# Optimization experiments

Measured on AMD Instinct MI355X. Metric: run time of the kernel, lower is better.

The kernel has to match this reference:

```python
import jax, jax.numpy as jnp
import numpy as np

FEATURE_DIM = 256
TEMP = 0.1
BASE_TEMP = 0.07
MAX_SAMPLES = 1024
SIM_THR = 0.7


def setup_inputs() -> dict:
    key = jax.random.key(0)
    ks = jax.random.split(key, 8)
    B, C, H, W = 4, FEATURE_DIM, 160, 160
    s = 1.0 / np.sqrt(C)
    return {
        'feats': jax.random.normal(ks[0], (B, C, H, W), jnp.float32),
        'labels': jax.random.randint(ks[1], (B, H, W), 0, 2).astype(jnp.int64),
        'superpixel_indice': jax.random.randint(ks[2], (B, H, W), 0, 200).astype(jnp.int64),
        'w1': jax.random.normal(ks[3], (C, C), jnp.float32) * s,
        'b1': jnp.zeros((C,), jnp.float32),
        'w2': jax.random.normal(ks[4], (C, C), jnp.float32) * s,
        'b2': jnp.zeros((C,), jnp.float32),
        'wa1': jax.random.normal(ks[5], (64, C), jnp.float32) * s,
        'ba1': jnp.zeros((64,), jnp.float32),
        'wa2': jax.random.normal(ks[6], (1, 64), jnp.float32) * (1.0 / 8.0),
        'ba2': jnp.zeros((1,), jnp.float32),
    }


def _per_sample(f, w, lab, sp):
    # f: (N, C) normalized proj feats, w: (N,) pixel weights, lab/sp: (N,) int
    valid = lab == 1
    # deterministic sample: stable-sort valid pixels to the front, take MAX_SAMPLES
    order = jnp.argsort(jnp.where(valid, 0, 1).astype(jnp.int32))
    idx = order[:MAX_SAMPLES]
    sel = valid[idx]                       # (S,) real-sample mask (pads if <S valid)
    tf = f[idx]                            # (S, C)
    tw = w[idx]                            # (S,)
    ts = sp[idx]                           # (S,)
    sim = tf @ tf.T                        # (S, S)
    S = MAX_SAMPLES
    eye = jnp.eye(S, dtype=bool)
    pos = (ts[:, None] == ts[None, :]) & (sim > SIM_THR)
    pos = pos & sel[:, None] & sel[None, :] & ~eye
    exp_sim = jnp.exp(sim / TEMP) * sel[None, :].astype(sim.dtype)
    denom = exp_sim.sum(axis=1)            # (S,)
    log_prob = sim / TEMP - jnp.log(jnp.where(denom > 0, denom, 1.0))[:, None]
    pw = tw[:, None] * tw[None, :]
    pwm = jnp.where(pos, pw, 0.0)
    psum = pwm.sum()
    loss = -(TEMP / BASE_TEMP) * (pwm * jnp.where(pos, log_prob, 0.0)).sum() / jnp.where(psum > 0, psum, 1.0)
    has = psum > 0
    return jnp.where(has, loss, 0.0), has


def reference(feats, labels, superpixel_indice, w1, b1, w2, b2, wa1, ba1, wa2, ba2):
    B, C, H, W = feats.shape
    x = jnp.transpose(feats, (0, 2, 3, 1)).reshape(B, H * W, C)  # (B, N, C)
    proj = jax.nn.relu(x @ w1.T + b1) @ w2.T + b2                # 1x1 convs == per-pixel matmul
    attn = jax.nn.sigmoid(jax.nn.relu(x @ wa1.T + ba1) @ wa2.T + ba2)[..., 0]  # (B, N)
    nrm = jnp.linalg.norm(proj, axis=-1, keepdims=True)
    fn = proj / jnp.maximum(nrm, 1e-12)
    lab = labels.reshape(B, -1)
    sp = superpixel_indice.reshape(B, -1)
    losses, flags = jax.vmap(_per_sample)(fn, attn, lab, sp)
    n = flags.sum().astype(jnp.float32)
    return jnp.where(n > 0, losses.sum() / jnp.maximum(n, 1.0), 0.0)
```

## Files before the change

### kernel.cpp

```cpp
#include <hip/hip_runtime.h>
#include <hip/hip_bf16.h>
#include <math.h>

#define NPIX   25600
#define CDIM   256
#define SSEL   1024
#define BATCH  4
#define NCHUNK 25
#define INV_T  10.0f
#define RATIO  1.4285714285714286f
#define THR    0.7f

typedef __attribute__((ext_vector_type(8))) short bf16x8;
typedef __attribute__((ext_vector_type(4))) float f32x4;
typedef unsigned short u16;

__device__ __forceinline__ u16 to_bf16(float v) {
  __hip_bfloat16 h = __float2bfloat16(v);
  return *reinterpret_cast<u16*>(&h);
}

__global__ __launch_bounds__(256) void pack_weights(
    const float* __restrict__ w1, const float* __restrict__ w2,
    const float* __restrict__ wa1, const int* __restrict__ labels,
    u16* __restrict__ w1b, u16* __restrict__ w2b, u16* __restrict__ wab,
    float* __restrict__ denom, float* __restrict__ Prow, float* __restrict__ Ssum,
    int* __restrict__ counts) {
  int t = threadIdx.x;
  int e = blockIdx.x * 256 + t;
  if (e < 65536) {
    w1b[e] = to_bf16(w1[e]);
    w2b[e] = to_bf16(w2[e]);
  }
  if (e < 16384) wab[e] = to_bf16(wa1[e]);
  if (e < BATCH * SSEL) { denom[e] = 0.f; Prow[e] = 0.f; }
  if (e < BATCH) Ssum[e] = 0.f;

  if (blockIdx.x < BATCH * NCHUNK) {
    int b = blockIdx.x / NCHUNK, ch = blockIdx.x % NCHUNK;
    const int* lab = labels + b * NPIX + ch * 1024;
    int local = 0;
#pragma unroll
    for (int qq = 0; qq < 4; ++qq) local += (lab[qq * 256 + t] == 1);
    for (int off = 32; off > 0; off >>= 1) local += __shfl_xor(local, off, 64);
    __shared__ int ws[4];
    if ((t & 63) == 0) ws[t >> 6] = local;
    __syncthreads();
    if (t == 0) counts[blockIdx.x] = ws[0] + ws[1] + ws[2] + ws[3];
  }
}

__global__ __launch_bounds__(1024) void select_scatter(
    const int* __restrict__ labels, const int* __restrict__ sp,
    const int* __restrict__ counts,
    int* __restrict__ idx, int* __restrict__ selv, int* __restrict__ tsp) {
  int b = blockIdx.x / NCHUNK, ch = blockIdx.x % NCHUNK;
  int t = threadIdx.x;
  __shared__ int cs[NCHUNK];
  __shared__ int wave_tot[16];
  if (t < NCHUNK) cs[t] = counts[b * NCHUNK + t];
  __syncthreads();
  int Vtot = 0, vbase = 0;
#pragma unroll
  for (int c = 0; c < NCHUNK; ++c) {
    int v = cs[c];
    Vtot += v;
    if (c < ch) vbase += v;
  }
  int ibase = ch * 1024 - vbase;

  int i = ch * 1024 + t;
  int isv = (labels[b * NPIX + i] == 1) ? 1 : 0;
  int lane = t & 63, wid = t >> 6;
  unsigned long long mv = __ballot(isv);
  int pv = __popcll(mv & ((1ull << lane) - 1ull));
  if (lane == 0) wave_tot[wid] = __popcll(mv);
  __syncthreads();
  for (int w = 0; w < wid; ++w) pv += wave_tot[w];
  int gslot = isv ? (vbase + pv) : (Vtot + ibase + (t - pv));
  if (gslot < SSEL) {
    idx [b * SSEL + gslot] = i;
    selv[b * SSEL + gslot] = isv;
    tsp [b * SSEL + gslot] = sp[b * NPIX + i];
  }
}

__global__ __launch_bounds__(256) void gather_cast(
    const float* __restrict__ feats, const int* __restrict__ idx,
    u16* __restrict__ xh) {
  int r0 = blockIdx.x * 4;
  int b  = r0 >> 10;
  int t  = threadIdx.x;
  __shared__ int ridx[4];
  if (t < 4) ridx[t] = idx[r0 + t];
  __syncthreads();
  const float* fb = feats + ((long)b * CDIM + t) * NPIX;
#pragma unroll
  for (int r = 0; r < 4; ++r) {
    xh[(long)(r0 + r) * CDIM + t] = to_bf16(fb[ridx[r]]);
  }
}

__global__ __launch_bounds__(256) void gemm1_kernel(
    const u16* __restrict__ xh, const u16* __restrict__ w1b,
    const u16* __restrict__ wab,
    const float* __restrict__ b1, const float* __restrict__ ba1,
    const float* __restrict__ wa2, const float* __restrict__ ba2,
    u16* __restrict__ hh, float* __restrict__ tw) {
  int n  = blockIdx.x;
  int i0 = blockIdx.y * 64;
  int t = threadIdx.x;
  int lane = t & 63, w = t >> 6, m = lane & 15, q = lane >> 4;
  bool attn = (n == 4);
  const u16* bsrc = attn ? wab : (w1b + n * 64 * 256);

  const u16* arow = xh + (i0 + w * 16 + m) * 256 + q * 8;
  const u16* brow = bsrc + m * 256 + q * 8;

  f32x4 acc[4];
#pragma unroll
  for (int nt = 0; nt < 4; ++nt) acc[nt] = {0.f, 0.f, 0.f, 0.f};

#pragma unroll
  for (int ks = 0; ks < 8; ++ks) {
    bf16x8 ah = *(const bf16x8*)&arow[ks * 32];
#pragma unroll
    for (int nt = 0; nt < 4; ++nt) {
      bf16x8 bh = *(const bf16x8*)&brow[nt * 16 * 256 + ks * 32];
      acc[nt] = __builtin_amdgcn_mfma_f32_16x16x32_bf16(ah, bh, acc[nt], 0, 0, 0);
    }
  }

  if (!attn) {
#pragma unroll
    for (int nt = 0; nt < 4; ++nt) {
      int col = n * 64 + nt * 16 + m;
      float bb = b1[col];
#pragma unroll
      for (int reg = 0; reg < 4; ++reg) {
        int row = i0 + w * 16 + q * 4 + reg;
        hh[row * 256 + col] = to_bf16(fmaxf(acc[nt][reg] + bb, 0.f));
      }
    }
  } else {
    float part[4] = {0.f, 0.f, 0.f, 0.f};
#pragma unroll
    for (int nt = 0; nt < 4; ++nt) {
      int ca = nt * 16 + m;
      float bb = ba1[ca], wv = wa2[ca];
#pragma unroll
      for (int reg = 0; reg < 4; ++reg)
        part[reg] += fmaxf(acc[nt][reg] + bb, 0.f) * wv;
    }
    for (int off = 8; off > 0; off >>= 1) {
#pragma unroll
      for (int reg = 0; reg < 4; ++reg)
        part[reg] += __shfl_xor(part[reg], off, 64);
    }
    if (m == 0) {
      float bb2 = ba2[0];
#pragma unroll
      for (int reg = 0; reg < 4; ++reg) {
        int row = i0 + w * 16 + q * 4 + reg;
        tw[row] = 1.f / (1.f + expf(-(part[reg] + bb2)));
      }
    }
  }
}

__global__ __launch_bounds__(256) void gemm2norm_kernel(
    const u16* __restrict__ hh, const u16* __restrict__ w2b,
    const float* __restrict__ b2, u16* __restrict__ fnb) {
  int i0 = blockIdx.x * 16;
  int t = threadIdx.x;
  int lane = t & 63, w = t >> 6, m = lane & 15, q = lane >> 4;

  const u16* arow = hh + (i0 + m) * 256 + q * 8;
  const u16* brow = w2b + (w * 64 + m) * 256 + q * 8;

  f32x4 acc[4];
#pragma unroll
  for (int nt = 0; nt < 4; ++nt) acc[nt] = {0.f, 0.f, 0.f, 0.f};

#pragma unroll
  for (int ks = 0; ks < 8; ++ks) {
    bf16x8 ah = *(const bf16x8*)&arow[ks * 32];
#pragma unroll
    for (int nt = 0; nt < 4; ++nt) {
      bf16x8 bh = *(const bf16x8*)&brow[nt * 16 * 256 + ks * 32];
      acc[nt] = __builtin_amdgcn_mfma_f32_16x16x32_bf16(ah, bh, acc[nt], 0, 0, 0);
    }
  }

  float ss[4] = {0.f, 0.f, 0.f, 0.f};
#pragma unroll
  for (int nt = 0; nt < 4; ++nt) {
    float bb = b2[w * 64 + nt * 16 + m];
#pragma unroll
    for (int reg = 0; reg < 4; ++reg) {
      float p = acc[nt][reg] + bb;
      acc[nt][reg] = p;
      ss[reg] += p * p;
    }
  }
  for (int off = 8; off > 0; off >>= 1) {
#pragma unroll
    for (int reg = 0; reg < 4; ++reg) ss[reg] += __shfl_xor(ss[reg], off, 64);
  }
  __shared__ float ssw[4][16];
  if (m == 0) {
#pragma unroll
    for (int reg = 0; reg < 4; ++reg) ssw[w][q * 4 + reg] = ss[reg];
  }
  __syncthreads();
#pragma unroll
  for (int nt = 0; nt < 4; ++nt) {
    int col = w * 64 + nt * 16 + m;
#pragma unroll
    for (int reg = 0; reg < 4; ++reg) {
      int r = q * 4 + reg;
      float tot = ssw[0][r] + ssw[1][r] + ssw[2][r] + ssw[3][r];
      float inv = 1.f / fmaxf(sqrtf(tot), 1e-12f);
      fnb[(i0 + r) * 256 + col] = to_bf16(acc[nt][reg] * inv);
    }
  }
}

__global__ __launch_bounds__(256) void sim_kernel(
    const u16* __restrict__ fnb, const float* __restrict__ tw,
    const int* __restrict__ selv, const int* __restrict__ tsp,
    float* __restrict__ denom, float* __restrict__ Prow, float* __restrict__ Ssum) {
  int b = blockIdx.y;
  int t = threadIdx.x;
  int lane = t & 63, w = t >> 6;
  int m = lane & 15, q = lane >> 4;

  int rem = blockIdx.x, ti = 0;
  while (rem >= (16 - ti)) { rem -= (16 - ti); ++ti; }
  int tj = ti + rem;
  int i0 = ti * 64, j0 = tj * 64;
  int base = b << 10;

  __shared__ float drl[64], Prl[64];
  __shared__ float dclw[4][64], Pclw[4][64];
  __shared__ float swv[4];

  const u16* arow = fnb + (base + i0 + w * 16 + m) * 256 + q * 8;
  const u16* brow = fnb + (base + j0 + m) * 256 + q * 8;

  f32x4 acc[4];
#pragma unroll
  for (int nt = 0; nt < 4; ++nt) acc[nt] = {0.f, 0.f, 0.f, 0.f};

#pragma unroll
  for (int ks = 0; ks < 8; ++ks) {
    bf16x8 ah = *(const bf16x8*)&arow[ks * 32];
#pragma unroll
    for (int nt = 0; nt < 4; ++nt) {
      bf16x8 bh = *(const bf16x8*)&brow[nt * 16 * 256 + ks * 32];
      acc[nt] = __builtin_amdgcn_mfma_f32_16x16x32_bf16(ah, bh, acc[nt], 0, 0, 0);
    }
  }

  bool diag = (ti == tj);
  int   gi[4], gj[4], si[4], sj[4], ci[4], cj[4];
  float twi[4], twj[4];
#pragma unroll
  for (int reg = 0; reg < 4; ++reg) {
    int i = i0 + w * 16 + q * 4 + reg;
    gi[reg] = i; twi[reg] = tw[base + i];
    si[reg] = selv[base + i]; ci[reg] = tsp[base + i];
  }
#pragma unroll
  for (int nt = 0; nt < 4; ++nt) {
    int j = j0 + nt * 16 + m;
    gj[nt] = j; twj[nt] = tw[base + j];
    sj[nt] = selv[base + j]; cj[nt] = tsp[base + j];
  }

  float dR[4] = {0, 0, 0, 0}, PR[4] = {0, 0, 0, 0};
  float dC[4] = {0, 0, 0, 0}, PC[4] = {0, 0, 0, 0};
  float Sp = 0.f;
#pragma unroll
  for (int nt = 0; nt < 4; ++nt) {
#pragma unroll
    for (int reg = 0; reg < 4; ++reg) {
      float s = acc[nt][reg];
      float e10 = __expf(s * INV_T);
      if (sj[nt]) dR[reg] += e10;
      if (si[reg]) dC[nt] += e10;
      if (si[reg] && sj[nt] && (ci[reg] == cj[nt]) && (s > THR) && (gi[reg] != gj[nt])) {
        float pw = twi[reg] * twj[nt];
        PR[reg] += pw;
        PC[nt] += pw;
        Sp += pw * s;
      }
    }
  }

  for (int off = 8; off > 0; off >>= 1) {
#pragma unroll
    for (int reg = 0; reg < 4; ++reg) {
      dR[reg] += __shfl_xor(dR[reg], off, 64);
      PR[reg] += __shfl_xor(PR[reg], off, 64);
    }
  }
  if (m == 0) {
#pragma unroll
    for (int reg = 0; reg < 4; ++reg) {
      drl[w * 16 + q * 4 + reg] = dR[reg];
      Prl[w * 16 + q * 4 + reg] = PR[reg];
    }
  }
  if (!diag) {
    for (int off = 32; off >= 16; off >>= 1) {
#pragma unroll
      for (int nt = 0; nt < 4; ++nt) {
        dC[nt] += __shfl_xor(dC[nt], off, 64);
        PC[nt] += __shfl_xor(PC[nt], off, 64);
      }
    }
    if (q == 0) {
#pragma unroll
      for (int nt = 0; nt < 4; ++nt) {
        dclw[w][nt * 16 + m] = dC[nt];
        Pclw[w][nt * 16 + m] = PC[nt];
      }
    }
  }
  for (int off = 32; off > 0; off >>= 1) Sp += __shfl_xor(Sp, off, 64);
  if (lane == 0) swv[w] = Sp;
  __syncthreads();

  if (t < 64) {
    atomicAdd(&denom[base + i0 + t], drl[t]);
    atomicAdd(&Prow [base + i0 + t], Prl[t]);
    if (!diag) {
      float dc = dclw[0][t] + dclw[1][t] + dclw[2][t] + dclw[3][t];
      float pc = Pclw[0][t] + Pclw[1][t] + Pclw[2][t] + Pclw[3][t];
      atomicAdd(&denom[base + j0 + t], dc);
      atomicAdd(&Prow [base + j0 + t], pc);
    }
  }
  if (t == 0) {
    float St = swv[0] + swv[1] + swv[2] + swv[3];
    atomicAdd(&Ssum[b], diag ? St : 2.f * St);
  }
}

__global__ __launch_bounds__(1024) void finalize_kernel(
    const float* __restrict__ denom, const float* __restrict__ Prow,
    const float* __restrict__ Ssum, float* __restrict__ out) {
  int t = threadIdx.x;
  int b = t >> 8, u = t & 255;
  float P = 0.f, L = 0.f;
#pragma unroll
  for (int q = 0; q < 4; ++q) {
    int s = u + q * 256;
    float p = Prow[b * SSEL + s];
    float D = denom[b * SSEL + s];
    P += p;
    L += p * logf(D > 0.f ? D : 1.f);
  }
  for (int off = 32; off > 0; off >>= 1) {
    P += __shfl_xor(P, off, 64);
    L += __shfl_xor(L, off, 64);
  }
  __shared__ float wP[16], wL[16];
  int lane = t & 63, w = t >> 6;
  if (lane == 0) { wP[w] = P; wL[w] = L; }
  __syncthreads();
  if (t == 0) {
    float total = 0.f, n = 0.f;
    for (int bb = 0; bb < BATCH; ++bb) {
      float psum = wP[4 * bb] + wP[4 * bb + 1] + wP[4 * bb + 2] + wP[4 * bb + 3];
      float lsum = wL[4 * bb] + wL[4 * bb + 1] + wL[4 * bb + 2] + wL[4 * bb + 3];
      if (psum > 0.f) {
        float wls = Ssum[bb] * INV_T - lsum;
        total += -RATIO * wls / psum;
        n += 1.f;
      }
    }
    out[0] = (n > 0.f) ? (total / n) : 0.f;
  }
}

extern "C" void kernel_launch(void* const* d_in, const int* in_sizes, int n_in,
                              void* d_out, int out_size, void* d_ws, size_t ws_size,
                              hipStream_t stream) {
  const float* feats = (const float*)d_in[0];
  const int*   labels = (const int*)d_in[1];
  const int*   sp     = (const int*)d_in[2];
  const float* w1  = (const float*)d_in[3];
  const float* b1  = (const float*)d_in[4];
  const float* w2  = (const float*)d_in[5];
  const float* b2  = (const float*)d_in[6];
  const float* wa1 = (const float*)d_in[7];
  const float* ba1 = (const float*)d_in[8];
  const float* wa2 = (const float*)d_in[9];
  const float* ba2 = (const float*)d_in[10];
  float* out = (float*)d_out;

  char* W = (char*)d_ws;
  u16* w1b = (u16*)W;               W += 65536 * 2;
  u16* w2b = (u16*)W;               W += 65536 * 2;
  u16* wab = (u16*)W;               W += 16384 * 2;
  u16* xh  = (u16*)W;               W += 1048576 * 2;
  u16* hh  = (u16*)W;               W += 1048576 * 2;
  u16* fnb = (u16*)W;               W += 1048576 * 2;
  float* tw   = (float*)W;          W += 4096 * 4;
  float* denom= (float*)W;          W += 4096 * 4;
  float* Prow = (float*)W;          W += 4096 * 4;
  float* Ssum = (float*)W;          W += 4 * 4;
  int*   idx  = (int*)W;            W += 4096 * 4;
  int*   selv = (int*)W;            W += 4096 * 4;
  int*   tsp  = (int*)W;            W += 4096 * 4;
  int*   counts = (int*)W;          W += 128 * 4;

  pack_weights<<<256, 256, 0, stream>>>(w1, w2, wa1, labels, w1b, w2b, wab,
                                        denom, Prow, Ssum, counts);
  select_scatter<<<BATCH * NCHUNK, 1024, 0, stream>>>(labels, sp, counts,
                                                      idx, selv, tsp);
  gather_cast<<<1024, 256, 0, stream>>>(feats, idx, xh);
  gemm1_kernel<<<dim3(5, 64), 256, 0, stream>>>(xh, w1b, wab, b1, ba1,
                                                wa2, ba2, hh, tw);
  gemm2norm_kernel<<<256, 256, 0, stream>>>(hh, w2b, b2, fnb);
  sim_kernel<<<dim3(136, BATCH), 256, 0, stream>>>(fnb, tw, selv, tsp,
                                                   denom, Prow, Ssum);
  finalize_kernel<<<1, 1024, 0, stream>>>(denom, Prow, Ssum, out);
}
```

Measured before the change: 201.0 us.

## Fuse select passes, fold finalize into sim via last-block, stage GEMM tiles in LDS

Merges the weight-pack/count kernel and the scatter kernel into one launch, where each block recounts all chunk label counts itself, so the intermediate counts buffer and one launch go away. The finalize kernel is folded into sim_kernel using a global done counter, so the last block to finish computes the loss. gemm1 and sim now stage 64-wide K slices of A and B into padded LDS tiles instead of issuing direct global fragment loads, and diagonal sim tiles reuse the A tile. In exchange, each select block reads 25x more labels, and the fused kernels add extra barriers and atomic traffic.

```diff
diff --git a/kernel.cpp b/kernel.cpp
--- a/kernel.cpp
+++ b/kernel.cpp
@@ -20,67 +20,68 @@
   return *reinterpret_cast<u16*>(&h);
 }
 
-__global__ __launch_bounds__(256) void pack_weights(
+__global__ __launch_bounds__(1024) void select_fused(
+    const int* __restrict__ labels, const int* __restrict__ sp,
     const float* __restrict__ w1, const float* __restrict__ w2,
-    const float* __restrict__ wa1, const int* __restrict__ labels,
+    const float* __restrict__ wa1,
     u16* __restrict__ w1b, u16* __restrict__ w2b, u16* __restrict__ wab,
+    int* __restrict__ idx, int* __restrict__ selv, int* __restrict__ tsp,
     float* __restrict__ denom, float* __restrict__ Prow, float* __restrict__ Ssum,
-    int* __restrict__ counts) {
+    unsigned int* __restrict__ done) {
+  int blk = blockIdx.x;
+  int b = blk / NCHUNK, ch = blk % NCHUNK;
   int t = threadIdx.x;
-  int e = blockIdx.x * 256 + t;
-  if (e < 65536) {
-    w1b[e] = to_bf16(w1[e]);
-    w2b[e] = to_bf16(w2[e]);
-  }
-  if (e < 16384) wab[e] = to_bf16(wa1[e]);
-  if (e < BATCH * SSEL) { denom[e] = 0.f; Prow[e] = 0.f; }
-  if (e < BATCH) Ssum[e] = 0.f;
-
-  if (blockIdx.x < BATCH * NCHUNK) {
-    int b = blockIdx.x / NCHUNK, ch = blockIdx.x % NCHUNK;
-    const int* lab = labels + b * NPIX + ch * 1024;
-    int local = 0;
-#pragma unroll
-    for (int qq = 0; qq < 4; ++qq) local += (lab[qq * 256 + t] == 1);
-    for (int off = 32; off > 0; off >>= 1) local += __shfl_xor(local, off, 64);
-    __shared__ int ws[4];
-    if ((t & 63) == 0) ws[t >> 6] = local;
-    __syncthreads();
-    if (t == 0) counts[blockIdx.x] = ws[0] + ws[1] + ws[2] + ws[3];
-  }
-}
-
-__global__ __launch_bounds__(1024) void select_scatter(
-    const int* __restrict__ labels, const int* __restrict__ sp,
-    const int* __restrict__ counts,
-    int* __restrict__ idx, int* __restrict__ selv, int* __restrict__ tsp) {
-  int b = blockIdx.x / NCHUNK, ch = blockIdx.x % NCHUNK;
-  int t = threadIdx.x;
-  __shared__ int cs[NCHUNK];
+  int lane = t & 63, wid = t >> 6;
+
+  int gid = blk * 1024 + t;
+  for (int e = gid; e < 147456; e += 102400) {
+    if (e < 65536)       w1b[e]          = to_bf16(w1[e]);
+    else if (e < 131072) w2b[e - 65536]  = to_bf16(w2[e - 65536]);
+    else                 wab[e - 131072] = to_bf16(wa1[e - 131072]);
+  }
+  if (gid < 4096) { denom[gid] = 0.f; Prow[gid] = 0.f; }
+  else if (gid < 4100) Ssum[gid - 4096] = 0.f;
+  else if (gid == 4100) *done = 0u;
+
+  __shared__ int cpart[NCHUNK][16];
+  __shared__ int csum[NCHUNK];
   __shared__ int wave_tot[16];
-  if (t < NCHUNK) cs[t] = counts[b * NCHUNK + t];
+  const int* lab = labels + b * NPIX;
+  int isv_my = 0;
+#pragma unroll
+  for (int c = 0; c < NCHUNK; ++c) {
+    int v = (lab[c * 1024 + t] == 1) ? 1 : 0;
+    if (c == ch) isv_my = v;
+    for (int off = 32; off > 0; off >>= 1) v += __shfl_xor(v, off, 64);
+    if (lane == 0) cpart[c][wid] = v;
+  }
+  __syncthreads();
+  if (t < NCHUNK) {
+    int s = 0;
+#pragma unroll
+    for (int w = 0; w < 16; ++w) s += cpart[t][w];
+    csum[t] = s;
+  }
   __syncthreads();
   int Vtot = 0, vbase = 0;
 #pragma unroll
   for (int c = 0; c < NCHUNK; ++c) {
-    int v = cs[c];
+    int v = csum[c];
     Vtot += v;
     if (c < ch) vbase += v;
   }
   int ibase = ch * 1024 - vbase;
 
-  int i = ch * 1024 + t;
-  int isv = (labels[b * NPIX + i] == 1) ? 1 : 0;
-  int lane = t & 63, wid = t >> 6;
-  unsigned long long mv = __ballot(isv);
+  unsigned long long mv = __ballot(isv_my);
   int pv = __popcll(mv & ((1ull << lane) - 1ull));
   if (lane == 0) wave_tot[wid] = __popcll(mv);
   __syncthreads();
   for (int w = 0; w < wid; ++w) pv += wave_tot[w];
-  int gslot = isv ? (vbase + pv) : (Vtot + ibase + (t - pv));
+  int i = ch * 1024 + t;
+  int gslot = isv_my ? (vbase + pv) : (Vtot + ibase + (t - pv));
   if (gslot < SSEL) {
     idx [b * SSEL + gslot] = i;
-    selv[b * SSEL + gslot] = isv;
+    selv[b * SSEL + gslot] = isv_my;
     tsp [b * SSEL + gslot] = sp[b * NPIX + i];
   }
 }
@@ -114,20 +115,33 @@
   bool attn = (n == 4);
   const u16* bsrc = attn ? wab : (w1b + n * 64 * 256);
 
-  const u16* arow = xh + (i0 + w * 16 + m) * 256 + q * 8;
-  const u16* brow = bsrc + m * 256 + q * 8;
+  __shared__ __align__(16) u16 Ah[64 * 72];
+  __shared__ __align__(16) u16 Bh[64 * 72];
 
   f32x4 acc[4];
 #pragma unroll
   for (int nt = 0; nt < 4; ++nt) acc[nt] = {0.f, 0.f, 0.f, 0.f};
 
-#pragma unroll
-  for (int ks = 0; ks < 8; ++ks) {
-    bf16x8 ah = *(const bf16x8*)&arow[ks * 32];
-#pragma unroll
-    for (int nt = 0; nt < 4; ++nt) {
-      bf16x8 bh = *(const bf16x8*)&brow[nt * 16 * 256 + ks * 32];
-      acc[nt] = __builtin_amdgcn_mfma_f32_16x16x32_bf16(ah, bh, acc[nt], 0, 0, 0);
+  for (int kk = 0; kk < 4; ++kk) {
+    __syncthreads();
+#pragma unroll
+    for (int p = 0; p < 2; ++p) {
+      int e = p * 256 + t;
+      int row = e >> 3, kg = e & 7;
+      int lo = row * 72 + kg * 8;
+      *(uint4*)&Ah[lo] = *(const uint4*)&xh[(i0 + row) * 256 + kk * 64 + kg * 8];
+      *(uint4*)&Bh[lo] = *(const uint4*)&bsrc[row * 256 + kk * 64 + kg * 8];
+    }
+    __syncthreads();
+#pragma unroll
+    for (int ks = 0; ks < 2; ++ks) {
+      int koff = ks * 32 + q * 8;
+      bf16x8 ah = *(const bf16x8*)&Ah[(w * 16 + m) * 72 + koff];
+#pragma unroll
+      for (int nt = 0; nt < 4; ++nt) {
+        bf16x8 bh = *(const bf16x8*)&Bh[(nt * 16 + m) * 72 + koff];
+        acc[nt] = __builtin_amdgcn_mfma_f32_16x16x32_bf16(ah, bh, acc[nt], 0, 0, 0);
+      }
     }
   }
 
@@ -229,7 +243,8 @@
 __global__ __launch_bounds__(256) void sim_kernel(
     const u16* __restrict__ fnb, const float* __restrict__ tw,
     const int* __restrict__ selv, const int* __restrict__ tsp,
-    float* __restrict__ denom, float* __restrict__ Prow, float* __restrict__ Ssum) {
+    float* __restrict__ denom, float* __restrict__ Prow, float* __restrict__ Ssum,
+    unsigned int* __restrict__ done, float* __restrict__ out) {
   int b = blockIdx.y;
   int t = threadIdx.x;
   int lane = t & 63, w = t >> 6;
@@ -238,31 +253,46 @@
   int rem = blockIdx.x, ti = 0;
   while (rem >= (16 - ti)) { rem -= (16 - ti); ++ti; }
   int tj = ti + rem;
+  bool diag = (ti == tj);
   int i0 = ti * 64, j0 = tj * 64;
   int base = b << 10;
 
+  __shared__ __align__(16) u16 Ah[64 * 72];
+  __shared__ __align__(16) u16 Bhh[64 * 72];
   __shared__ float drl[64], Prl[64];
   __shared__ float dclw[4][64], Pclw[4][64];
   __shared__ float swv[4];
 
-  const u16* arow = fnb + (base + i0 + w * 16 + m) * 256 + q * 8;
-  const u16* brow = fnb + (base + j0 + m) * 256 + q * 8;
+  const u16* Bh = diag ? Ah : Bhh;
 
   f32x4 acc[4];
 #pragma unroll
   for (int nt = 0; nt < 4; ++nt) acc[nt] = {0.f, 0.f, 0.f, 0.f};
 
-#pragma unroll
-  for (int ks = 0; ks < 8; ++ks) {
-    bf16x8 ah = *(const bf16x8*)&arow[ks * 32];
-#pragma unroll
-    for (int nt = 0; nt < 4; ++nt) {
-      bf16x8 bh = *(const bf16x8*)&brow[nt * 16 * 256 + ks * 32];
-      acc[nt] = __builtin_amdgcn_mfma_f32_16x16x32_bf16(ah, bh, acc[nt], 0, 0, 0);
-    }
-  }
-
-  bool diag = (ti == tj);
+  for (int kk = 0; kk < 4; ++kk) {
+    __syncthreads();
+#pragma unroll
+    for (int p = 0; p < 2; ++p) {
+      int e = p * 256 + t;
+      int row = e >> 3, kg = e & 7;
+      int lo = row * 72 + kg * 8;
+      *(uint4*)&Ah[lo] = *(const uint4*)&fnb[(base + i0 + row) * 256 + kk * 64 + kg * 8];
+      if (!diag)
+        *(uint4*)&Bhh[lo] = *(const uint4*)&fnb[(base + j0 + row) * 256 + kk * 64 + kg * 8];
+    }
+    __syncthreads();
+#pragma unroll
+    for (int ks = 0; ks < 2; ++ks) {
+      int koff = ks * 32 + q * 8;
+      bf16x8 ah = *(const bf16x8*)&Ah[(w * 16 + m) * 72 + koff];
+#pragma unroll
+      for (int nt = 0; nt < 4; ++nt) {
+        bf16x8 bh = *(const bf16x8*)&Bh[(nt * 16 + m) * 72 + koff];
+        acc[nt] = __builtin_amdgcn_mfma_f32_16x16x32_bf16(ah, bh, acc[nt], 0, 0, 0);
+      }
+    }
+  }
+
   int   gi[4], gj[4], si[4], sj[4], ci[4], cj[4];
   float twi[4], twj[4];
 #pragma unroll
@@ -346,43 +376,45 @@
     float St = swv[0] + swv[1] + swv[2] + swv[3];
     atomicAdd(&Ssum[b], diag ? St : 2.f * St);
   }
-}
-
-__global__ __launch_bounds__(1024) void finalize_kernel(
-    const float* __restrict__ denom, const float* __restrict__ Prow,
-    const float* __restrict__ Ssum, float* __restrict__ out) {
-  int t = threadIdx.x;
-  int b = t >> 8, u = t & 255;
-  float P = 0.f, L = 0.f;
-#pragma unroll
-  for (int q = 0; q < 4; ++q) {
-    int s = u + q * 256;
-    float p = Prow[b * SSEL + s];
-    float D = denom[b * SSEL + s];
-    P += p;
-    L += p * logf(D > 0.f ? D : 1.f);
-  }
-  for (int off = 32; off > 0; off >>= 1) {
-    P += __shfl_xor(P, off, 64);
-    L += __shfl_xor(L, off, 64);
-  }
-  __shared__ float wP[16], wL[16];
-  int lane = t & 63, w = t >> 6;
-  if (lane == 0) { wP[w] = P; wL[w] = L; }
-  __syncthreads();
-  if (t == 0) {
-    float total = 0.f, n = 0.f;
-    for (int bb = 0; bb < BATCH; ++bb) {
-      float psum = wP[4 * bb] + wP[4 * bb + 1] + wP[4 * bb + 2] + wP[4 * bb + 3];
-      float lsum = wL[4 * bb] + wL[4 * bb + 1] + wL[4 * bb + 2] + wL[4 * bb + 3];
+
+  __shared__ int lastf;
+  __shared__ float rP[4], rL[4];
+  __threadfence();
+  if (t == 0)
+    lastf = (atomicAdd(done, 1u) == (136u * BATCH - 1u)) ? 1 : 0;
+  __syncthreads();
+  if (!lastf) return;
+
+  float total = 0.f, ncnt = 0.f;
+  for (int bb = 0; bb < BATCH; ++bb) {
+    float P = 0.f, L = 0.f;
+    for (int k = t; k < SSEL; k += 256) {
+      float p = __hip_atomic_load(&Prow[bb * SSEL + k], __ATOMIC_RELAXED,
+                                  __HIP_MEMORY_SCOPE_AGENT);
+      float D = __hip_atomic_load(&denom[bb * SSEL + k], __ATOMIC_RELAXED,
+                                  __HIP_MEMORY_SCOPE_AGENT);
+      P += p;
+      L += p * logf(D > 0.f ? D : 1.f);
+    }
+    for (int off = 32; off > 0; off >>= 1) {
+      P += __shfl_xor(P, off, 64);
+      L += __shfl_xor(L, off, 64);
+    }
+    if (lane == 0) { rP[w] = P; rL[w] = L; }
+    __syncthreads();
+    if (t == 0) {
+      float psum = rP[0] + rP[1] + rP[2] + rP[3];
+      float lsum = rL[0] + rL[1] + rL[2] + rL[3];
+      float Sb = __hip_atomic_load(&Ssum[bb], __ATOMIC_RELAXED,
+                                   __HIP_MEMORY_SCOPE_AGENT);
       if (psum > 0.f) {
-        float wls = Ssum[bb] * INV_T - lsum;
-        total += -RATIO * wls / psum;
-        n += 1.f;
-      }
-    }
-    out[0] = (n > 0.f) ? (total / n) : 0.f;
-  }
+        total += -RATIO * (Sb * INV_T - lsum) / psum;
+        ncnt += 1.f;
+      }
+    }
+    __syncthreads();
+  }
+  if (t == 0) out[0] = (ncnt > 0.f) ? (total / ncnt) : 0.f;
 }
 
 extern "C" void kernel_launch(void* const* d_in, const int* in_sizes, int n_in,
@@ -415,17 +447,15 @@
   int*   idx  = (int*)W;            W += 4096 * 4;
   int*   selv = (int*)W;            W += 4096 * 4;
   int*   tsp  = (int*)W;            W += 4096 * 4;
-  int*   counts = (int*)W;          W += 128 * 4;
-
-  pack_weights<<<256, 256, 0, stream>>>(w1, w2, wa1, labels, w1b, w2b, wab,
-                                        denom, Prow, Ssum, counts);
-  select_scatter<<<BATCH * NCHUNK, 1024, 0, stream>>>(labels, sp, counts,
-                                                      idx, selv, tsp);
+  unsigned int* done = (unsigned int*)W; W += 4;
+
+  select_fused<<<BATCH * NCHUNK, 1024, 0, stream>>>(
+      labels, sp, w1, w2, wa1, w1b, w2b, wab,
+      idx, selv, tsp, denom, Prow, Ssum, done);
   gather_cast<<<1024, 256, 0, stream>>>(feats, idx, xh);
   gemm1_kernel<<<dim3(5, 64), 256, 0, stream>>>(xh, w1b, wab, b1, ba1,
                                                 wa2, ba2, hh, tw);
   gemm2norm_kernel<<<256, 256, 0, stream>>>(hh, w2b, b2, fnb);
   sim_kernel<<<dim3(136, BATCH), 256, 0, stream>>>(fnb, tw, selv, tsp,
-                                                   denom, Prow, Ssum);
-  finalize_kernel<<<1, 1024, 0, stream>>>(denom, Prow, Ssum, out);
-}
+                                                   denom, Prow, Ssum, done, out);
+}
```

New measurement: 235.8 us. +17.3%, slower.
